# Kernel tuning notes

Hardware: AMD Instinct MI355X
Metric: run time of the kernel (lower is better)

## Reference

```python
import jax, jax.numpy as jnp
import numpy as np

H, W, NUM_BUCKETS, NUM_LOOPS = 512, 512, 6, 4
N_DET, N_SAMPLES, BATCH = 4096, 128, 4


def setup_inputs() -> dict:
    key = jax.random.key(0)
    k1, k2, k3, k4 = jax.random.split(key, 4)
    det_indices = jax.random.uniform(k1, (N_DET, N_SAMPLES, 2), dtype=jnp.float32)
    det_indices = det_indices * jnp.array([W - 1, H - 1], jnp.float32)  # (x, y) coords
    refinement = jax.random.normal(k2, (BATCH, 2 * NUM_BUCKETS, H, W), dtype=jnp.float32)
    sampling = jax.random.uniform(k3, (N_SAMPLES,), dtype=jnp.float32)
    b = jax.random.randint(k4, (N_DET,), 0, BATCH, dtype=jnp.int64 if jax.config.jax_enable_x64 else jnp.int32)
    return {"det_indices": det_indices, "refinement": refinement, "sampling": sampling,
            "b": b, "num_loops": NUM_LOOPS, "num_buckets": NUM_BUCKETS, "height": H, "width": W}


def _bucket_weight(idx_f, base):
    # triangular weight: 1 - |idx - base|, zero outside unit distance; detached in torch
    d = jnp.abs(idx_f - base)
    return jax.lax.stop_gradient(jnp.where(d > 1.0, 0.0, 1.0 - d))


def reference(det_indices, refinement, sampling, b, num_loops, num_buckets, height, width):
    base = sampling * num_buckets               # [S]
    base_int = jnp.floor(base).astype(jnp.int32)
    det = det_indices
    for _ in range(num_loops):
        det = jnp.round(jax.lax.stop_gradient(det))
        det = jnp.stack([jnp.clip(det[..., 0], 0, width - 1),
                         jnp.clip(det[..., 1], 0, height - 1)], -1)
        idx = det.astype(jnp.int32)
        xi, yi = idx[..., 0], idx[..., 1]       # [N, S]
        responses = jnp.zeros_like(det)
        for off in (-1, 0, 1):
            bi = (base_int + off) % num_buckets                       # [S]
            w = _bucket_weight((base_int + off).astype(base.dtype), base)  # [S]
            bckt = jnp.stack([bi * 2, bi * 2 + 1], -1)                # [S, 2] channel pairs
            # gather -> [N, S, 2]
            cur = refinement[b[:, None, None], bckt[None, :, :], yi[..., None], xi[..., None]]
            responses = responses + cur * w[None, :, None]
        det = det + responses
    return det
```

## Files before the change

### kernel.cpp

```cpp
#include <hip/hip_runtime.h>

#define HREF   512
#define WREF   512
#define NBUCK  6
#define NLOOP  4
#define NDET   4096
#define NSAMP  128
#define BATCH  4
#define PLANE  (HREF * WREF)
#define NCHAN  (2 * NBUCK)
#define RECSZ  16

__global__ __launch_bounds__(256) void CPN_transpose_kernel(
    const float* __restrict__ ref, float* __restrict__ ws)
{
    const int t = blockIdx.x * blockDim.x + threadIdx.x;
    const int b = t >> 18;
    const int p = t & (PLANE - 1);

    const float* src = ref + (size_t)b * NCHAN * PLANE + p;
    float* dst = ws + ((size_t)t << 4);

    float v[RECSZ];
    #pragma unroll
    for (int c = 0; c < NCHAN; ++c) v[c] = src[(size_t)c << 18];
    #pragma unroll
    for (int c = NCHAN; c < RECSZ; ++c) v[c] = 0.0f;

    #pragma unroll
    for (int c = 0; c < RECSZ; c += 4)
        *(float4*)(dst + c) = make_float4(v[c], v[c+1], v[c+2], v[c+3]);
}

__global__ __launch_bounds__(256) void CPN_4492535791617_kernel(
    const float* __restrict__ det_in,
    const float* __restrict__ ws,
    const float* __restrict__ sampling,
    const int*   __restrict__ bsel,
    float*       __restrict__ out)
{
    const int tid = blockIdx.x * blockDim.x + threadIdx.x;
    const int s = tid & (NSAMP - 1);
    const int d = tid >> 7;

    float2 det = ((const float2*)det_in)[tid];
    const int bb = bsel[d];

    const float base = sampling[s] * (float)NBUCK;
    const float bf   = floorf(base);
    const float frac = base - bf;
    const float w0   = 1.0f - frac;
    const float w1   = frac;
    int bi = (int)bf;
    if (bi >= NBUCK) bi -= NBUCK;
    if (bi < 0)      bi  = 0;
    int bj = bi + 1; if (bj >= NBUCK) bj -= NBUCK;

    const float* slab = ws + ((size_t)bb << 18 << 4);

    #pragma unroll
    for (int l = 0; l < NLOOP; ++l) {
        float x = rintf(det.x);
        float y = rintf(det.y);
        x = fminf(fmaxf(x, 0.0f), (float)(WREF - 1));
        y = fminf(fmaxf(y, 0.0f), (float)(HREF - 1));
        const int p = (int)y * WREF + (int)x;

        const float* rec = slab + ((size_t)p << 4);
        const float2 ga = *(const float2*)(rec + 2 * bi);
        const float2 gb = *(const float2*)(rec + 2 * bj);

        det.x = x + (w0 * ga.x + w1 * gb.x);
        det.y = y + (w0 * ga.y + w1 * gb.y);
    }

    ((float2*)out)[tid] = det;
}

__global__ __launch_bounds__(256) void CPN_fallback_kernel(
    const float* __restrict__ det_in,
    const float* __restrict__ refinement,
    const float* __restrict__ sampling,
    const int*   __restrict__ bsel,
    float*       __restrict__ out)
{
    const int tid = blockIdx.x * blockDim.x + threadIdx.x;
    const int s = tid & (NSAMP - 1);
    const int d = tid >> 7;

    float2 det = ((const float2*)det_in)[tid];
    const int bb = bsel[d];

    const float base = sampling[s] * (float)NBUCK;
    const float bf   = floorf(base);
    const float frac = base - bf;
    const float w0   = 1.0f - frac;
    const float w1   = frac;
    int bi = (int)bf;
    if (bi >= NBUCK) bi -= NBUCK;
    if (bi < 0)      bi  = 0;
    int bj = bi + 1; if (bj >= NBUCK) bj -= NBUCK;

    const size_t plane = (size_t)PLANE;
    const float* slab = refinement + (size_t)bb * NCHAN * plane;
    const float* c0 = slab + (size_t)(2 * bi)     * plane;
    const float* c1 = slab + (size_t)(2 * bi + 1) * plane;
    const float* c2 = slab + (size_t)(2 * bj)     * plane;
    const float* c3 = slab + (size_t)(2 * bj + 1) * plane;

    #pragma unroll
    for (int l = 0; l < NLOOP; ++l) {
        float x = rintf(det.x);
        float y = rintf(det.y);
        x = fminf(fmaxf(x, 0.0f), (float)(WREF - 1));
        y = fminf(fmaxf(y, 0.0f), (float)(HREF - 1));
        const int p = (int)y * WREF + (int)x;
        det.x = x + (w0 * c0[p] + w1 * c2[p]);
        det.y = y + (w0 * c1[p] + w1 * c3[p]);
    }

    ((float2*)out)[tid] = det;
}

extern "C" void kernel_launch(void* const* d_in, const int* in_sizes, int n_in,
                              void* d_out, int out_size, void* d_ws, size_t ws_size,
                              hipStream_t stream) {
    const float* det_indices = (const float*)d_in[0];
    const float* refinement  = (const float*)d_in[1];
    const float* sampling    = (const float*)d_in[2];
    const int*   b           = (const int*)  d_in[3];
    float* out = (float*)d_out;

    const size_t need = (size_t)BATCH * PLANE * RECSZ * sizeof(float);

    const int total = NDET * NSAMP;
    const int block = 256;
    const int grid  = total / block;

    if (ws_size >= need) {
        float* ws = (float*)d_ws;
        const int tp_total = BATCH * PLANE;
        CPN_transpose_kernel<<<tp_total / block, block, 0, stream>>>(refinement, ws);
        CPN_4492535791617_kernel<<<grid, block, 0, stream>>>(
            det_indices, ws, sampling, b, out);
    } else {
        CPN_fallback_kernel<<<grid, block, 0, stream>>>(
            det_indices, refinement, sampling, b, out);
    }
}
```

Measured before the change: 139.5 us.

## Group detections by batch and map blocks to XCDs for L2 locality

Adds a single-block partition kernel that sorts detection indices by batch id into a permutation array. The main kernel then remaps each block id so that consecutive ranges of same-batch work land on the same XCD, and reads det/out through the permutation. The goal is for each XCD's L2 to mostly serve one batch's 16MB transposed slab instead of all four, raising cache hit rates on the random gathers. It costs an extra serial launch and an indirection load per thread.

```diff
diff --git a/kernel.cpp b/kernel.cpp
--- a/kernel.cpp
+++ b/kernel.cpp
@@ -10,6 +10,30 @@
 #define PLANE  (HREF * WREF)
 #define NCHAN  (2 * NBUCK)
 #define RECSZ  16
+#define NPAIR  (NDET * NSAMP)
+#define NXCD   8
+
+__global__ __launch_bounds__(256) void CPN_partition_kernel(
+    const int* __restrict__ bsel, int* __restrict__ perm)
+{
+    __shared__ int cnt[BATCH];
+    __shared__ int off[BATCH];
+    const int tid = threadIdx.x;
+    if (tid < BATCH) cnt[tid] = 0;
+    __syncthreads();
+    for (int d = tid; d < NDET; d += 256) atomicAdd(&cnt[bsel[d]], 1);
+    __syncthreads();
+    if (tid == 0) {
+        int acc = 0;
+        for (int q = 0; q < BATCH; ++q) { off[q] = acc; acc += cnt[q]; }
+    }
+    __syncthreads();
+    for (int d = tid; d < NDET; d += 256) {
+        const int q = bsel[d];
+        const int slot = atomicAdd(&off[q], 1);
+        perm[slot] = d | (q << 16);
+    }
+}
 
 __global__ __launch_bounds__(256) void CPN_transpose_kernel(
     const float* __restrict__ ref, float* __restrict__ ws)
@@ -36,15 +60,18 @@
     const float* __restrict__ det_in,
     const float* __restrict__ ws,
     const float* __restrict__ sampling,
-    const int*   __restrict__ bsel,
+    const int*   __restrict__ perm,
     float*       __restrict__ out)
 {
-    const int tid = blockIdx.x * blockDim.x + threadIdx.x;
-    const int s = tid & (NSAMP - 1);
-    const int d = tid >> 7;
+    const int r = (blockIdx.x & (NXCD - 1)) * (2048 / NXCD) + (blockIdx.x >> 3);
+    const int j = r * 256 + threadIdx.x;
+    const int s = j & (NSAMP - 1);
+    const int pe = perm[j >> 7];
+    const int d  = pe & 0xFFFF;
+    const int bb = pe >> 16;
+    const int tid = d * NSAMP + s;
 
     float2 det = ((const float2*)det_in)[tid];
-    const int bb = bsel[d];
 
     const float base = sampling[s] * (float)NBUCK;
     const float bf   = floorf(base);
@@ -131,18 +158,20 @@
     const int*   b           = (const int*)  d_in[3];
     float* out = (float*)d_out;
 
-    const size_t need = (size_t)BATCH * PLANE * RECSZ * sizeof(float);
+    const size_t rec_bytes = (size_t)BATCH * PLANE * RECSZ * sizeof(float);
+    const size_t need = rec_bytes + NDET * sizeof(int);
 
-    const int total = NDET * NSAMP;
     const int block = 256;
-    const int grid  = total / block;
+    const int grid  = NPAIR / block;
 
     if (ws_size >= need) {
-        float* ws = (float*)d_ws;
+        float* ws  = (float*)d_ws;
+        int* perm  = (int*)((char*)d_ws + rec_bytes);
+        CPN_partition_kernel<<<1, block, 0, stream>>>(b, perm);
         const int tp_total = BATCH * PLANE;
         CPN_transpose_kernel<<<tp_total / block, block, 0, stream>>>(refinement, ws);
         CPN_4492535791617_kernel<<<grid, block, 0, stream>>>(
-            det_indices, ws, sampling, b, out);
+            det_indices, ws, sampling, perm, out);
     } else {
         CPN_fallback_kernel<<<grid, block, 0, stream>>>(
             det_indices, refinement, sampling, b, out);
```

New measurement: 144.4 us. 1.04x slower.
